# Optimization experiments

Hardware: AMD Instinct MI355X
Metric: run time of the kernel (lower is better)

The kernel has to match this reference:

```python
import jax, jax.numpy as jnp
import numpy as np
from jax import lax

HEADS = 8
EPS = 1e-5
B, HP, N = 16, 16, 256  # batch, patches per side, tokens


def _ln(x, w, b):
    m = x.mean(-1, keepdims=True)
    v = ((x - m) ** 2).mean(-1, keepdims=True)
    return (x - m) / jnp.sqrt(v + EPS) * w + b


def _mlp_block(x, n2w, n2b, f1w, f1b, f2w, f2b):
    h = _ln(x, n2w, n2b)
    h = jax.nn.gelu(h @ f1w.T + f1b, approximate=False)  # torch nn.GELU = exact erf
    return x + (h @ f2w.T + f2b)


def _stem_stage(x, params):
    def step(c, p):
        return _mlp_block(c, *p), None
    x, _ = lax.scan(step, x, params)
    return x


def _patch_merge(x, nw, nb, rw):
    # x: [B, N, s, s, C] -> [B, N, s/2, s/2, 2C]
    x = jnp.concatenate([x[..., 0::2, 0::2, :], x[..., 1::2, 0::2, :],
                         x[..., 0::2, 1::2, :], x[..., 1::2, 1::2, :]], axis=-1)
    return _ln(x, nw, nb) @ rw.T


def _main_block(x, p, rpe_index):
    n1w, n1b, qkvw, qkvb, rpb, pw, pb, n2w, n2b, f1w, f1b, f2w, f2b = p
    Bc, Nc, C = x.shape
    Dh = C // HEADS
    h = _ln(x, n1w, n1b)
    qkv = (h @ qkvw.T + qkvb).reshape(Bc, Nc, 3, HEADS, Dh)
    q, k, v = jnp.moveaxis(qkv, 2, 0)
    attn = jnp.einsum('bnhd,bmhd->bhnm', q * (Dh ** -0.5), k)
    # learned relative position bias gathered per (query, key) pair
    bias = rpb[rpe_index].reshape(Nc, Nc, HEADS).transpose(2, 0, 1)  # [H,N,N]
    attn = jax.nn.softmax((attn + bias[None]).astype(jnp.float32), axis=-1).astype(x.dtype)
    o = jnp.einsum('bhnm,bmhd->bnhd', attn, v).reshape(Bc, Nc, C)
    x = x + (o @ pw.T + pb)
    return _mlp_block(x, n2w, n2b, f1w, f1b, f2w, f2b)


def _forward(x, patch_w, patch_b, pnorm_w, pnorm_b,
             s0_n2w, s0_n2b, s0_fc1w, s0_fc1b, s0_fc2w, s0_fc2b,
             m0_nw, m0_nb, m0_rw,
             s1_n2w, s1_n2b, s1_fc1w, s1_fc1b, s1_fc2w, s1_fc2b,
             m1_nw, m1_nb, m1_rw, pos_embed,
             mb_n1w, mb_n1b, mb_qkvw, mb_qkvb, mb_rpb, mb_projw, mb_projb,
             mb_n2w, mb_n2b, mb_fc1w, mb_fc1b, mb_fc2w, mb_fc2b,
             fnorm_w, fnorm_b, rpe_index):
    Bc = x.shape[0]
    # PatchEmbed: 4x4/stride4 conv, regroup into [B, 256 patches, 4, 4, 128]
    h = lax.conv_general_dilated(x, patch_w, (4, 4), 'VALID',
                                 dimension_numbers=('NCHW', 'OIHW', 'NCHW'))
    h = h + patch_b[None, :, None, None]  # [B,128,64,64]
    h = h.reshape(Bc, 128, HP, 4, HP, 4).transpose(0, 2, 4, 3, 5, 1).reshape(Bc, N, 4, 4, 128)
    h = _ln(h, pnorm_w, pnorm_b)
    # stem stage 0 (8 MLP-only blocks, dim 128) + merge -> dim 256
    h = _stem_stage(h, (s0_n2w, s0_n2b, s0_fc1w, s0_fc1b, s0_fc2w, s0_fc2b))
    h = _patch_merge(h, m0_nw, m0_nb, m0_rw)  # [B,256,2,2,256]
    # stem stage 1 (8 MLP-only blocks, dim 256) + merge -> dim 512
    h = _stem_stage(h, (s1_n2w, s1_n2b, s1_fc1w, s1_fc1b, s1_fc2w, s1_fc2b))
    h = _patch_merge(h, m1_nw, m1_nb, m1_rw)  # [B,256,1,1,512]
    h = h[..., 0, 0, :] + pos_embed  # [B,256,512]
    # 20 main attention blocks with RPE
    def step(c, p):
        return _main_block(c, p, rpe_index), None
    h, _ = lax.scan(step, h, (mb_n1w, mb_n1b, mb_qkvw, mb_qkvb, mb_rpb,
                              mb_projw, mb_projb, mb_n2w, mb_n2b,
                              mb_fc1w, mb_fc1b, mb_fc2w, mb_fc2b))
    return _ln(h, fnorm_w, fnorm_b)


def _rpe_index():
    coords = np.stack(np.meshgrid(np.arange(HP), np.arange(HP), indexing='ij')).reshape(2, -1)
    rel = (coords[:, :, None] - coords[:, None, :]).transpose(1, 2, 0) + (HP - 1)
    return jnp.asarray((rel[..., 0] * (2 * HP - 1) + rel[..., 1]).reshape(-1), jnp.int32)


def setup_inputs() -> dict:
    key = jax.random.key(0)
    ks = iter(jax.random.split(key, 64))
    w = lambda shape: jax.random.normal(next(ks), shape, jnp.float32) * 0.02
    return {
        'x': jax.random.normal(next(ks), (B, 3, 256, 256), jnp.float32),
        'patch_w': w((128, 3, 4, 4)), 'patch_b': jnp.zeros(128),
        'pnorm_w': jnp.ones(128), 'pnorm_b': jnp.zeros(128),
        's0_n2w': jnp.ones((8, 128)), 's0_n2b': jnp.zeros((8, 128)),
        's0_fc1w': w((8, 384, 128)), 's0_fc1b': jnp.zeros((8, 384)),
        's0_fc2w': w((8, 128, 384)), 's0_fc2b': jnp.zeros((8, 128)),
        'm0_nw': jnp.ones(512), 'm0_nb': jnp.zeros(512), 'm0_rw': w((256, 512)),
        's1_n2w': jnp.ones((8, 256)), 's1_n2b': jnp.zeros((8, 256)),
        's1_fc1w': w((8, 768, 256)), 's1_fc1b': jnp.zeros((8, 768)),
        's1_fc2w': w((8, 256, 768)), 's1_fc2b': jnp.zeros((8, 256)),
        'm1_nw': jnp.ones(1024), 'm1_nb': jnp.zeros(1024), 'm1_rw': w((512, 1024)),
        'pos_embed': w((1, N, 512)),
        'mb_n1w': jnp.ones((20, 512)), 'mb_n1b': jnp.zeros((20, 512)),
        'mb_qkvw': w((20, 1536, 512)), 'mb_qkvb': jnp.zeros((20, 1536)),
        'mb_rpb': w((20, 961, 8)),
        'mb_projw': w((20, 512, 512)), 'mb_projb': jnp.zeros((20, 512)),
        'mb_n2w': jnp.ones((20, 512)), 'mb_n2b': jnp.zeros((20, 512)),
        'mb_fc1w': w((20, 2048, 512)), 'mb_fc1b': jnp.zeros((20, 2048)),
        'mb_fc2w': w((20, 512, 2048)), 'mb_fc2b': jnp.zeros((20, 512)),
        'fnorm_w': jnp.ones(512), 'fnorm_b': jnp.zeros(512),
        'rpe_index': _rpe_index(),
    }


def reference(x, patch_w, patch_b, pnorm_w, pnorm_b,
              s0_n2w, s0_n2b, s0_fc1w, s0_fc1b, s0_fc2w, s0_fc2b,
              m0_nw, m0_nb, m0_rw,
              s1_n2w, s1_n2b, s1_fc1w, s1_fc1b, s1_fc2w, s1_fc2b,
              m1_nw, m1_nb, m1_rw, pos_embed,
              mb_n1w, mb_n1b, mb_qkvw, mb_qkvb, mb_rpb, mb_projw, mb_projb,
              mb_n2w, mb_n2b, mb_fc1w, mb_fc1b, mb_fc2w, mb_fc2b,
              fnorm_w, fnorm_b, rpe_index):
    return _forward(x, patch_w, patch_b, pnorm_w, pnorm_b,
                    s0_n2w, s0_n2b, s0_fc1w, s0_fc1b, s0_fc2w, s0_fc2b,
                    m0_nw, m0_nb, m0_rw,
                    s1_n2w, s1_n2b, s1_fc1w, s1_fc1b, s1_fc2w, s1_fc2b,
                    m1_nw, m1_nb, m1_rw, pos_embed,
                    mb_n1w, mb_n1b, mb_qkvw, mb_qkvb, mb_rpb, mb_projw, mb_projb,
                    mb_n2w, mb_n2b, mb_fc1w, mb_fc1b, mb_fc2w, mb_fc2b,
                    fnorm_w, fnorm_b, rpe_index)
```

## Files before the change

kernel.cpp:

```cpp
#include <hip/hip_runtime.h>
#include <math.h>

#define EPSV 1e-5f

typedef __attribute__((ext_vector_type(8))) short bf16x8;
typedef __attribute__((ext_vector_type(4))) float f32x4;
typedef unsigned short ushort;

__device__ inline ushort f2bf(float x) {
  unsigned u = __builtin_bit_cast(unsigned, x);
  u += 0x7FFFu + ((u >> 16) & 1u);
  return (ushort)(u >> 16);
}

#define GLOAD16(lptr, gptr)                                              \
  __builtin_amdgcn_global_load_lds(                                      \
      (const __attribute__((address_space(1))) unsigned int*)(gptr),     \
      (__attribute__((address_space(3))) unsigned int*)(lptr), 16, 0, 0)

__global__ __launch_bounds__(256) void convh_kernel(
    const float* __restrict__ in, ushort* __restrict__ hi, int n4) {
  int i = blockIdx.x * 256 + threadIdx.x;
  if (i >= n4) return;
  float4 v = ((const float4*)in)[i];
  float vv[4] = {v.x, v.y, v.z, v.w};
  unsigned hw[4];
#pragma unroll
  for (int e = 0; e < 4; ++e) hw[e] = f2bf(vv[e]);
  ((uint2*)hi)[i] = make_uint2(hw[0] | (hw[1] << 16), hw[2] | (hw[3] << 16));
}

__global__ __launch_bounds__(256) void convmain_kernel(
    const float* __restrict__ src, ushort* __restrict__ dst, int perLayer4,
    int dstOff4, int n4) {
  int i = blockIdx.x * 256 + threadIdx.x;
  if (i >= n4) return;
  int l = i / perLayer4;
  int r = i - l * perLayer4;
  float4 v = ((const float4*)src)[i];
  float vv[4] = {v.x, v.y, v.z, v.w};
  unsigned hw[4];
#pragma unroll
  for (int e = 0; e < 4; ++e) hw[e] = f2bf(vv[e]);
  ((uint2*)dst)[(size_t)l * 786432 + dstOff4 + r] =
      make_uint2(hw[0] | (hw[1] << 16), hw[2] | (hw[3] << 16));
}

__global__ __launch_bounds__(256) void patch_ln2_kernel(
    const float* __restrict__ x, const float* __restrict__ pw,
    const float* __restrict__ pbias, const float* __restrict__ nw,
    const float* __restrict__ nb, float* __restrict__ out) {
  int bid = blockIdx.x;
  int b = bid >> 8, n = bid & 255;
  int py = (n >> 4) * 16, px0 = (n & 15) * 16;
  __shared__ float xin[3][16][16];
  __shared__ float wls[128][52];
  __shared__ float pbs[128];
  int tid = threadIdx.x;
  if (tid < 192) {
    int ci = tid / 64, rr = (tid % 64) >> 2, c4 = tid & 3;
    const float* src =
        x + ((size_t)(b * 3 + ci) * 256 + (py + rr)) * 256 + px0 + c4 * 4;
    *(float4*)&xin[ci][rr][c4 * 4] = *(const float4*)src;
  }
  for (int idx = tid; idx < 6144; idx += 256) {
    int c = idx / 48, q = idx % 48;
    wls[c][q] = pw[c * 48 + q];
  }
  if (tid < 128) pbs[tid] = pbias[tid];
  __syncthreads();

  int tt = tid >> 4, cg = tid & 15;
  int ii = tt >> 2, jj = tt & 3;
  float xv[48];
#pragma unroll
  for (int ci = 0; ci < 3; ++ci)
#pragma unroll
    for (int dy = 0; dy < 4; ++dy)
#pragma unroll
      for (int dx = 0; dx < 4; ++dx)
        xv[ci * 16 + dy * 4 + dx] = xin[ci][ii * 4 + dy][jj * 4 + dx];

  float o[8];
#pragma unroll
  for (int e = 0; e < 8; ++e) {
    int c = cg + e * 16;
    float a = pbs[c];
#pragma unroll
    for (int q4 = 0; q4 < 12; ++q4) {
      float4 w4 = *(const float4*)&wls[c][q4 * 4];
      a += w4.x * xv[q4 * 4] + w4.y * xv[q4 * 4 + 1] + w4.z * xv[q4 * 4 + 2] +
           w4.w * xv[q4 * 4 + 3];
    }
    o[e] = a;
  }
  float s = 0.f;
#pragma unroll
  for (int e = 0; e < 8; ++e) s += o[e];
#pragma unroll
  for (int off = 8; off > 0; off >>= 1) s += __shfl_xor(s, off, 16);
  float mean = s * (1.0f / 128.0f);
  float sq = 0.f;
#pragma unroll
  for (int e = 0; e < 8; ++e) {
    float d = o[e] - mean;
    sq += d * d;
  }
#pragma unroll
  for (int off = 8; off > 0; off >>= 1) sq += __shfl_xor(sq, off, 16);
  float rstd = rsqrtf(sq * (1.0f / 128.0f) + EPSV);
  size_t base = ((size_t)bid * 16 + tt) * 128;
#pragma unroll
  for (int e = 0; e < 8; ++e) {
    int c = cg + e * 16;
    out[base + c] = (o[e] - mean) * rstd * nw[c] + nb[c];
  }
}

template <int C>
__global__ __launch_bounds__(256) void lnC_kernel(
    const float* __restrict__ X, const float* __restrict__ w,
    const float* __restrict__ bb, ushort* __restrict__ outH) {
  constexpr int NV = C / 64;
  int wave = threadIdx.x >> 6, lane = threadIdx.x & 63;
  int row = blockIdx.x * 4 + wave;
  const float* xr = X + (size_t)row * C + lane * NV;
  float v[NV];
  if (NV == 2) {
    float2 t2 = *(const float2*)xr;
    v[0] = t2.x; v[1] = t2.y;
  } else {
#pragma unroll
    for (int q = 0; q < NV; q += 4) {
      float4 t4 = *(const float4*)(xr + q);
      v[q] = t4.x; v[q + 1] = t4.y; v[q + 2] = t4.z; v[q + 3] = t4.w;
    }
  }
  float s = 0.f;
#pragma unroll
  for (int q = 0; q < NV; ++q) s += v[q];
#pragma unroll
  for (int o = 32; o > 0; o >>= 1) s += __shfl_xor(s, o, 64);
  float mean = s * (1.0f / C);
  float sq = 0.f;
#pragma unroll
  for (int q = 0; q < NV; ++q) {
    float d = v[q] - mean;
    sq += d * d;
  }
#pragma unroll
  for (int o = 32; o > 0; o >>= 1) sq += __shfl_xor(sq, o, 64);
  float rstd = rsqrtf(sq * (1.0f / C) + EPSV);
#pragma unroll
  for (int q = 0; q < NV; ++q) {
    int c = lane * NV + q;
    outH[(size_t)row * C + c] = f2bf((v[q] - mean) * rstd * w[c] + bb[c]);
  }
}

template <int MODE>
__global__ __launch_bounds__(256) void merge_ln_kernel(
    const float* __restrict__ Xin, const float* __restrict__ nw,
    const float* __restrict__ nb, ushort* __restrict__ outH) {
  constexpr int CM = MODE ? 1024 : 512;
  constexpr int NE = CM / 256;
  int ot = blockIdx.x;
  int tid = threadIdx.x;
  __shared__ float redA[4];
  __shared__ float redB[4];

  float v[NE];
#pragma unroll
  for (int e = 0; e < NE; ++e) {
    int cp = tid + e * 256;
    if (MODE == 0) {
      int b = ot >> 10, r = ot & 1023;
      int n = r >> 2, di = (r >> 1) & 1, dj = r & 1;
      int q = cp >> 7, c = cp & 127;
      int i = 2 * di + (q & 1), j = 2 * dj + (q >> 1);
      v[e] = Xin[((b * 256 + n) * 16 + i * 4 + j) * 128 + c];
    } else {
      int b = ot >> 8, n = ot & 255;
      int q = cp >> 8, c = cp & 255;
      int di = q & 1, dj = q >> 1;
      v[e] = Xin[((b * 256 + n) * 4 + di * 2 + dj) * 256 + c];
    }
  }
  float s = 0.f;
#pragma unroll
  for (int e = 0; e < NE; ++e) s += v[e];
#pragma unroll
  for (int o = 32; o > 0; o >>= 1) s += __shfl_xor(s, o, 64);
  if ((tid & 63) == 0) redA[tid >> 6] = s;
  __syncthreads();
  float mean = (redA[0] + redA[1] + redA[2] + redA[3]) * (1.0f / CM);
  float sq = 0.f;
#pragma unroll
  for (int e = 0; e < NE; ++e) {
    float d = v[e] - mean;
    sq += d * d;
  }
#pragma unroll
  for (int o = 32; o > 0; o >>= 1) sq += __shfl_xor(sq, o, 64);
  if ((tid & 63) == 0) redB[tid >> 6] = sq;
  __syncthreads();
  float var = (redB[0] + redB[1] + redB[2] + redB[3]) * (1.0f / CM);
  float rstd = rsqrtf(var + EPSV);
#pragma unroll
  for (int e = 0; e < NE; ++e) {
    int cp = tid + e * 256;
    outH[(size_t)ot * CM + cp] = f2bf((v[e] - mean) * rstd * nw[cp] + nb[cp]);
  }
}

template <int EP, int BM>
__global__ __launch_bounds__(256) void mgemm4_kernel(
    const ushort* __restrict__ Ah, const ushort* __restrict__ Wh,
    const float* __restrict__ bias, const float* __restrict__ extra,
    float* __restrict__ outF, ushort* __restrict__ outH, int M, int N, int K) {
  constexpr int NI = BM / 32;
  constexpr int ASH = BM * 64;
  constexpr int LSZ = (ASH + 8192 > BM * 136) ? (ASH + 8192) : (BM * 136);
  __shared__ __align__(16) ushort Lds[LSZ];
  int nb = N >> 7;
  int bx = blockIdx.x % nb, by = blockIdx.x / nb;
  int tid = threadIdx.x;
  int wv = tid >> 6, lane = tid & 63;
  int srow = tid >> 3;
  int scol = ((tid & 7) ^ (srow & 7)) << 3;
  const ushort* aS = Ah + (size_t)(by * BM + srow) * K + scol;
  const ushort* wS = Wh + (size_t)(bx * 128 + srow) * K + scol;
  ushort* dA = Lds + wv * 512;
  ushort* dW = Lds + ASH + wv * 512;

  int wm = (wv >> 1) * (BM / 2), wn = (wv & 1) * 64;
  int fr = lane & 15, fq = lane >> 4;
  int rsw = fr & 7;

  f32x4 acc[NI][4];
#pragma unroll
  for (int i = 0; i < NI; ++i)
#pragma unroll
    for (int j = 0; j < 4; ++j) acc[i][j] = {0.f, 0.f, 0.f, 0.f};

  for (int k0 = 0; k0 < K; k0 += 64) {
#pragma unroll
    for (int q = 0; q < BM / 32; ++q)
      GLOAD16(dA + q * 2048, aS + (size_t)q * 32 * K + k0);
#pragma unroll
    for (int q = 0; q < 4; ++q)
      GLOAD16(dW + q * 2048, wS + (size_t)q * 32 * K + k0);
    __syncthreads();

#pragma unroll
    for (int kh = 0; kh < 2; ++kh) {
      bf16x8 fa[NI], fb[4];
#pragma unroll
      for (int i = 0; i < NI; ++i) {
        int row = wm + i * 16 + fr;
        fa[i] = *(const bf16x8*)(Lds + row * 64 + ((((kh << 2) + fq) ^ rsw) << 3));
      }
#pragma unroll
      for (int j = 0; j < 4; ++j) {
        int row = wn + j * 16 + fr;
        fb[j] = *(const bf16x8*)(Lds + ASH + row * 64 +
                                 ((((kh << 2) + fq) ^ rsw) << 3));
      }
#pragma unroll
      for (int i = 0; i < NI; ++i)
#pragma unroll
        for (int j = 0; j < 4; ++j)
          acc[i][j] = __builtin_amdgcn_mfma_f32_16x16x32_bf16(fa[i], fb[j],
                                                              acc[i][j], 0, 0,
                                                              0);
    }
    __syncthreads();
  }

  int row0 = by * BM;
  int col0 = bx * 128;
  if (EP == 3 || EP == 4) {
    ushort* LdsO = Lds;
#pragma unroll
    for (int j = 0; j < 4; ++j) {
      int col = wn + j * 16 + fr;
      float bvv = bias ? bias[col0 + col] : 0.f;
      bool sc = (EP == 4) && (col0 + col < 512);
#pragma unroll
      for (int i = 0; i < NI; ++i) {
#pragma unroll
        for (int e = 0; e < 4; ++e) {
          int rl = wm + i * 16 + fq * 4 + e;
          float o = acc[i][j][e] + bvv;
          if (EP == 3)
            o = 0.5f * o * (1.0f + erff(o * 0.70710678118654752f));
          else if (sc)
            o *= 0.125f;
          LdsO[rl * 136 + col] = f2bf(o);
        }
      }
    }
    __syncthreads();
#pragma unroll
    for (int p = 0; p < BM / 16; ++p) {
      int ch = p * 256 + tid;
      int r = ch >> 4, cc = (ch & 15) * 8;
      *(uint4*)&outH[(size_t)(row0 + r) * N + col0 + cc] =
          *(const uint4*)&LdsO[r * 136 + cc];
    }
  } else {
    float* LdsF = (float*)Lds;
    int strip = wv >> 1;
#pragma unroll
    for (int i = 0; i < NI; ++i) {
#pragma unroll
      for (int j = 0; j < 4; ++j) {
        int col = wn + j * 16 + fr;
        float bvv = bias ? bias[col0 + col] : 0.f;
#pragma unroll
        for (int e = 0; e < 4; ++e)
          LdsF[(strip * 16 + fq * 4 + e) * 136 + col] = acc[i][j][e] + bvv;
      }
      __syncthreads();
#pragma unroll
      for (int p = 0; p < 4; ++p) {
        int c = p * 256 + tid;
        int st = c >> 9;
        int rem = c & 511;
        int r = rem >> 5, cc = (rem & 31) * 4;
        int grow = row0 + st * (BM / 2) + i * 16 + r;
        float4 v = *(const float4*)&LdsF[(st * 16 + r) * 136 + cc];
        if (EP == 1) {
          float4 e4 =
              *(const float4*)&extra[(size_t)(grow & 255) * N + col0 + cc];
          v.x += e4.x; v.y += e4.y; v.z += e4.z; v.w += e4.w;
        } else if (EP == 2) {
          float4 e4 = *(const float4*)&extra[(size_t)grow * N + col0 + cc];
          v.x += e4.x; v.y += e4.y; v.z += e4.z; v.w += e4.w;
        }
        *(float4*)&outF[(size_t)grow * N + col0 + cc] = v;
      }
      __syncthreads();
    }
  }
}

__global__ __launch_bounds__(256) void attn_fused2_kernel(
    const ushort* __restrict__ qkvh, const float* __restrict__ rpb,
    const int* __restrict__ rpe, ushort* __restrict__ outH) {
  int bid = blockIdx.x;
  int qc = bid & 3, bh = bid >> 2;
  int b = bh >> 3, h = bh & 7;
  int n0 = qc * 64;
  int tid = threadIdx.x;
  int wv = tid >> 6, lane = tid & 63;
  int fr = lane & 15, fq = lane >> 4;
  __shared__ __align__(16) ushort Qs[64 * 64];
  __shared__ __align__(16) ushort Ks[256 * 64];
  __shared__ __align__(16) ushort Vt[64 * 256];
  __shared__ float rpbh[961];
  __shared__ float red[64][4];

  int srow = tid >> 3;
  int sc = ((tid & 7) ^ (srow & 7)) << 3;
  const ushort* Qg = qkvh + (size_t)(b * 256 + n0 + srow) * 1536 + h * 64 + sc;
  GLOAD16(Qs + wv * 512, Qg);
  GLOAD16(Qs + 2048 + wv * 512, Qg + (size_t)32 * 1536);
  const ushort* Kg = qkvh + (size_t)(b * 256 + srow) * 1536 + 512 + h * 64 + sc;
#pragma unroll
  for (int q = 0; q < 8; ++q)
    GLOAD16(Ks + q * 2048 + wv * 512, Kg + (size_t)q * 32 * 1536);
#pragma unroll
  for (int pass = 0; pass < 4; ++pass) {
    int m = pass * 64 + (tid >> 2);
    int sg = (tid & 3) * 16;
    const ushort* Vg = qkvh + (size_t)(b * 256 + m) * 1536 + 1024 + h * 64 + sg;
    ushort tmp[16];
    *(uint4*)tmp = *(const uint4*)Vg;
    *(uint4*)(tmp + 8) = *(const uint4*)(Vg + 8);
    int ch = m >> 3, ml = m & 7;
#pragma unroll
    for (int e = 0; e < 16; ++e) {
      int d = sg + e;
      int cs = (ch & 24) | ((ch & 7) ^ (d & 7));
      Vt[d * 256 + cs * 8 + ml] = tmp[e];
    }
  }
  for (int i = tid; i < 961; i += 256) rpbh[i] = rpb[i * 8 + h];
  __syncthreads();

  f32x4 acc[4][4];
#pragma unroll
  for (int i = 0; i < 4; ++i)
#pragma unroll
    for (int j = 0; j < 4; ++j) acc[i][j] = {0.f, 0.f, 0.f, 0.f};
#pragma unroll
  for (int kh = 0; kh < 2; ++kh) {
    bf16x8 fa[4], fb[4];
#pragma unroll
    for (int i = 0; i < 4; ++i) {
      int row = i * 16 + fr;
      fa[i] = *(const bf16x8*)(Qs + row * 64 +
                               ((((kh << 2) + fq) ^ (row & 7)) << 3));
    }
#pragma unroll
    for (int j = 0; j < 4; ++j) {
      int row = wv * 64 + j * 16 + fr;
      fb[j] = *(const bf16x8*)(Ks + row * 64 +
                               ((((kh << 2) + fq) ^ (row & 7)) << 3));
    }
#pragma unroll
    for (int i = 0; i < 4; ++i)
#pragma unroll
      for (int j = 0; j < 4; ++j)
        acc[i][j] = __builtin_amdgcn_mfma_f32_16x16x32_bf16(fa[i], fb[j],
                                                            acc[i][j], 0, 0, 0);
  }

  float sreg[4][4][4];
#pragma unroll
  for (int i = 0; i < 4; ++i)
#pragma unroll
    for (int e = 0; e < 4; ++e) {
      int n = n0 + i * 16 + fq * 4 + e;
#pragma unroll
      for (int j = 0; j < 4; ++j) {
        int m = wv * 64 + j * 16 + fr;
        sreg[i][j][e] = acc[i][j][e] + rpbh[rpe[n * 256 + m]];
      }
    }

  float rmax[4][4];
#pragma unroll
  for (int i = 0; i < 4; ++i)
#pragma unroll
    for (int e = 0; e < 4; ++e) {
      float mx = fmaxf(fmaxf(sreg[i][0][e], sreg[i][1][e]),
                       fmaxf(sreg[i][2][e], sreg[i][3][e]));
#pragma unroll
      for (int o = 8; o > 0; o >>= 1) mx = fmaxf(mx, __shfl_xor(mx, o, 16));
      if (fr == 0) red[i * 16 + fq * 4 + e][wv] = mx;
    }
  __syncthreads();
#pragma unroll
  for (int i = 0; i < 4; ++i)
#pragma unroll
    for (int e = 0; e < 4; ++e) {
      int row = i * 16 + fq * 4 + e;
      rmax[i][e] = fmaxf(fmaxf(red[row][0], red[row][1]),
                         fmaxf(red[row][2], red[row][3]));
    }
  __syncthreads();
  float rinv[4][4];
#pragma unroll
  for (int i = 0; i < 4; ++i)
#pragma unroll
    for (int e = 0; e < 4; ++e) {
      float sm = 0.f;
#pragma unroll
      for (int j = 0; j < 4; ++j) {
        sreg[i][j][e] = expf(sreg[i][j][e] - rmax[i][e]);
        sm += sreg[i][j][e];
      }
#pragma unroll
      for (int o = 8; o > 0; o >>= 1) sm += __shfl_xor(sm, o, 16);
      if (fr == 0) red[i * 16 + fq * 4 + e][wv] = sm;
    }
  __syncthreads();
#pragma unroll
  for (int i = 0; i < 4; ++i)
#pragma unroll
    for (int e = 0; e < 4; ++e) {
      int row = i * 16 + fq * 4 + e;
      rinv[i][e] =
          1.0f / (red[row][0] + red[row][1] + red[row][2] + red[row][3]);
    }
  ushort* Ps = Ks;
#pragma unroll
  for (int i = 0; i < 4; ++i)
#pragma unroll
    for (int e = 0; e < 4; ++e) {
      int qrow = i * 16 + fq * 4 + e;
#pragma unroll
      for (int j = 0; j < 4; ++j) {
        int m = wv * 64 + j * 16 + fr;
        int ch = m >> 3, t = m & 7;
        int cs = (ch & 24) | ((ch & 7) ^ (qrow & 7));
        Ps[qrow * 256 + cs * 8 + t] = f2bf(sreg[i][j][e] * rinv[i][e]);
      }
    }
  __syncthreads();

  f32x4 pacc[4];
#pragma unroll
  for (int i = 0; i < 4; ++i) pacc[i] = {0.f, 0.f, 0.f, 0.f};
  int dbase = wv * 16;
#pragma unroll
  for (int ks = 0; ks < 8; ++ks) {
    int ch = (ks << 2) + fq;
    bf16x8 fb;
    {
      int row = dbase + fr;
      int cs = (ch & 24) | ((ch & 7) ^ (row & 7));
      fb = *(const bf16x8*)(Vt + row * 256 + cs * 8);
    }
    bf16x8 fa[4];
#pragma unroll
    for (int i = 0; i < 4; ++i) {
      int row = i * 16 + fr;
      int cs = (ch & 24) | ((ch & 7) ^ (row & 7));
      fa[i] = *(const bf16x8*)(Ps + row * 256 + cs * 8);
    }
#pragma unroll
    for (int i = 0; i < 4; ++i)
      pacc[i] = __builtin_amdgcn_mfma_f32_16x16x32_bf16(fa[i], fb, pacc[i], 0,
                                                        0, 0);
  }
#pragma unroll
  for (int i = 0; i < 4; ++i)
#pragma unroll
    for (int e = 0; e < 4; ++e) {
      int q = i * 16 + fq * 4 + e;
      outH[(size_t)(b * 256 + n0 + q) * 512 + h * 64 + dbase + fr] =
          f2bf(pacc[i][e]);
    }
}

template <int HL>
__global__ __launch_bounds__(256) void ln512_kernel(
    const float* __restrict__ X, const float* __restrict__ w,
    const float* __restrict__ bb, float* __restrict__ outF,
    ushort* __restrict__ outH) {
  int row = blockIdx.x * 4 + (threadIdx.x >> 6);
  int t = threadIdx.x & 63;
  const float4* xr = (const float4*)(X + (size_t)row * 512);
  float4 v0 = xr[t * 2], v1 = xr[t * 2 + 1];
  float s = v0.x + v0.y + v0.z + v0.w + v1.x + v1.y + v1.z + v1.w;
#pragma unroll
  for (int o = 32; o > 0; o >>= 1) s += __shfl_xor(s, o, 64);
  float mean = s * (1.0f / 512.0f);
  float dv[8] = {v0.x - mean, v0.y - mean, v0.z - mean, v0.w - mean,
                 v1.x - mean, v1.y - mean, v1.z - mean, v1.w - mean};
  float sq = 0.f;
#pragma unroll
  for (int e = 0; e < 8; ++e) sq += dv[e] * dv[e];
#pragma unroll
  for (int o = 32; o > 0; o >>= 1) sq += __shfl_xor(sq, o, 64);
  float rstd = rsqrtf(sq * (1.0f / 512.0f) + EPSV);
  int c = t * 8;
  float ov[8];
#pragma unroll
  for (int e = 0; e < 8; ++e) ov[e] = dv[e] * rstd * w[c + e] + bb[c + e];
  if (HL == 0) {
    float4 o0 = {ov[0], ov[1], ov[2], ov[3]};
    float4 o1 = {ov[4], ov[5], ov[6], ov[7]};
    ((float4*)(outF + (size_t)row * 512))[t * 2] = o0;
    ((float4*)(outF + (size_t)row * 512))[t * 2 + 1] = o1;
  } else {
    __align__(16) ushort h8[8];
#pragma unroll
    for (int e = 0; e < 8; ++e) h8[e] = f2bf(ov[e]);
    *(bf16x8*)(outH + (size_t)row * 512 + c) = *(bf16x8*)h8;
  }
}

extern "C" void kernel_launch(void* const* d_in, const int* in_sizes, int n_in,
                              void* d_out, int out_size, void* d_ws,
                              size_t ws_size, hipStream_t stream) {
  const float* x = (const float*)d_in[0];
  const float* patch_w = (const float*)d_in[1];
  const float* patch_b = (const float*)d_in[2];
  const float* pnorm_w = (const float*)d_in[3];
  const float* pnorm_b = (const float*)d_in[4];
  const float* s0_n2w = (const float*)d_in[5];
  const float* s0_n2b = (const float*)d_in[6];
  const float* s0_f1w = (const float*)d_in[7];
  const float* s0_f1b = (const float*)d_in[8];
  const float* s0_f2w = (const float*)d_in[9];
  const float* s0_f2b = (const float*)d_in[10];
  const float* m0_nw = (const float*)d_in[11];
  const float* m0_nb = (const float*)d_in[12];
  const float* m0_rw = (const float*)d_in[13];
  const float* s1_n2w = (const float*)d_in[14];
  const float* s1_n2b = (const float*)d_in[15];
  const float* s1_f1w = (const float*)d_in[16];
  const float* s1_f1b = (const float*)d_in[17];
  const float* s1_f2w = (const float*)d_in[18];
  const float* s1_f2b = (const float*)d_in[19];
  const float* m1_nw = (const float*)d_in[20];
  const float* m1_nb = (const float*)d_in[21];
  const float* m1_rw = (const float*)d_in[22];
  const float* pos_embed = (const float*)d_in[23];
  const float* mb_n1w = (const float*)d_in[24];
  const float* mb_n1b = (const float*)d_in[25];
  const float* mb_qkvw = (const float*)d_in[26];
  const float* mb_qkvb = (const float*)d_in[27];
  const float* mb_rpb = (const float*)d_in[28];
  const float* mb_projw = (const float*)d_in[29];
  const float* mb_projb = (const float*)d_in[30];
  const float* mb_n2w = (const float*)d_in[31];
  const float* mb_n2b = (const float*)d_in[32];
  const float* mb_f1w = (const float*)d_in[33];
  const float* mb_f1b = (const float*)d_in[34];
  const float* mb_f2w = (const float*)d_in[35];
  const float* mb_f2b = (const float*)d_in[36];
  const float* fnorm_w = (const float*)d_in[37];
  const float* fnorm_b = (const float*)d_in[38];
  const int* rpe = (const int*)d_in[39];

  float* Xa = (float*)d_ws;
  ushort* BufB = (ushort*)(Xa + 8388608);
  ushort* BufC = (ushort*)(Xa + 12582912);
  ushort* Qkvh = BufC;
  ushort* F1h = BufC + 14680064;
  ushort* Wall = (ushort*)(Xa + 25165824);
  ushort* WallBig = (ushort*)(Xa + 27262976);

#define CONVH(src, cnt, dh)                                              \
  convh_kernel<<<((cnt) / 4 + 255) / 256, 256, 0, stream>>>(src, dh, (cnt) / 4)

  convmain_kernel<<<(20 * 196608 + 255) / 256, 256, 0, stream>>>(
      mb_qkvw, WallBig, 196608, 0, 20 * 196608);
  convmain_kernel<<<(20 * 65536 + 255) / 256, 256, 0, stream>>>(
      mb_projw, WallBig, 65536, 196608, 20 * 65536);
  convmain_kernel<<<(20 * 262144 + 255) / 256, 256, 0, stream>>>(
      mb_f1w, WallBig, 262144, 262144, 20 * 262144);
  convmain_kernel<<<(20 * 262144 + 255) / 256, 256, 0, stream>>>(
      mb_f2w, WallBig, 262144, 524288, 20 * 262144);

  patch_ln2_kernel<<<4096, 256, 0, stream>>>(x, patch_w, patch_b, pnorm_w,
                                             pnorm_b, Xa);

  CONVH(s0_f1w, 8 * 49152, Wall);
  CONVH(s0_f2w, 8 * 49152, Wall + 393216);
  for (int i = 0; i < 8; ++i) {
    lnC_kernel<128><<<65536 / 4, 256, 0, stream>>>(Xa, s0_n2w + i * 128,
                                                   s0_n2b + i * 128, BufB);
    mgemm4_kernel<3, 128><<<(65536 / 128) * (384 / 128), 256, 0, stream>>>(
        BufB, Wall + i * 49152, s0_f1b + i * 384, nullptr, nullptr, BufC,
        65536, 384, 128);
    mgemm4_kernel<2, 64><<<(65536 / 64) * (128 / 128), 256, 0, stream>>>(
        BufC, Wall + 393216 + i * 49152, s0_f2b + i * 128, Xa, Xa, nullptr,
        65536, 128, 384);
  }
  merge_ln_kernel<0><<<16384, 256, 0, stream>>>(Xa, m0_nw, m0_nb, BufB);
  CONVH(m0_rw, 131072, Wall);
  mgemm4_kernel<0, 128><<<(16384 / 128) * (256 / 128), 256, 0, stream>>>(
      BufB, Wall, nullptr, nullptr, Xa, nullptr, 16384, 256, 512);

  CONVH(s1_f1w, 8 * 196608, Wall);
  CONVH(s1_f2w, 8 * 196608, Wall + 1572864);
  for (int i = 0; i < 8; ++i) {
    lnC_kernel<256><<<16384 / 4, 256, 0, stream>>>(Xa, s1_n2w + i * 256,
                                                   s1_n2b + i * 256, BufB);
    mgemm4_kernel<3, 128><<<(16384 / 128) * (768 / 128), 256, 0, stream>>>(
        BufB, Wall + i * 196608, s1_f1b + i * 768, nullptr, nullptr, BufC,
        16384, 768, 256);
    mgemm4_kernel<2, 64><<<(16384 / 64) * (256 / 128), 256, 0, stream>>>(
        BufC, Wall + 1572864 + i * 196608, s1_f2b + i * 256, Xa, Xa, nullptr,
        16384, 256, 768);
  }
  merge_ln_kernel<1><<<4096, 256, 0, stream>>>(Xa, m1_nw, m1_nb, BufB);
  CONVH(m1_rw, 524288, Wall);
  mgemm4_kernel<1, 64><<<(4096 / 64) * (512 / 128), 256, 0, stream>>>(
      BufB, Wall, nullptr, pos_embed, Xa, nullptr, 4096, 512, 1024);

  for (int l = 0; l < 20; ++l) {
    ushort* Wl = WallBig + (size_t)l * 3145728;
    ln512_kernel<1><<<1024, 256, 0, stream>>>(Xa, mb_n1w + l * 512,
                                              mb_n1b + l * 512, nullptr, BufB);
    mgemm4_kernel<4, 64><<<(4096 / 64) * (1536 / 128), 256, 0, stream>>>(
        BufB, Wl, mb_qkvb + l * 1536, nullptr, nullptr, Qkvh, 4096, 1536,
        512);
    attn_fused2_kernel<<<512, 256, 0, stream>>>(Qkvh, mb_rpb + l * 7688, rpe,
                                                BufB);
    mgemm4_kernel<2, 64><<<(4096 / 64) * (512 / 128), 256, 0, stream>>>(
        BufB, Wl + 786432, mb_projb + l * 512, Xa, Xa, nullptr, 4096, 512,
        512);
    ln512_kernel<1><<<1024, 256, 0, stream>>>(Xa, mb_n2w + l * 512,
                                              mb_n2b + l * 512, nullptr, BufB);
    mgemm4_kernel<3, 128><<<(4096 / 128) * (2048 / 128), 256, 0, stream>>>(
        BufB, Wl + 1048576, mb_f1b + l * 2048, nullptr, nullptr, F1h, 4096,
        2048, 512);
    mgemm4_kernel<2, 64><<<(4096 / 64) * (512 / 128), 256, 0, stream>>>(
        F1h, Wl + 2097152, mb_f2b + l * 512, Xa, Xa, nullptr, 4096, 512,
        2048);
  }
  ln512_kernel<0><<<1024, 256, 0, stream>>>(Xa, fnorm_w, fnorm_b,
                                            (float*)d_out, nullptr);
}
```

Before: 3.531 ms.

## Fuse stem LayerNorm into FC1 GEMM with GELU epilogue

Replaces the separate LayerNorm kernel plus FC1 GEMM in both stem stages with a new kernel. It loads the fp32 activation tile into LDS, computes per-row mean and rstd, and applies normalization with bf16 conversion on the fly while building MFMA A-fragments. This removes the bf16 intermediate write and read and one launch per block. The cost is that each N-tile recomputes LN and re-reads fp32 X (3x or 6x redundancy), uses more LDS with smaller BM tiles, and does per-element conversion in the inner loop.

```diff
diff --git a/kernel.cpp b/kernel.cpp
--- a/kernel.cpp
+++ b/kernel.cpp
@@ -114,47 +114,6 @@
   for (int e = 0; e < 8; ++e) {
     int c = cg + e * 16;
     out[base + c] = (o[e] - mean) * rstd * nw[c] + nb[c];
-  }
-}
-
-template <int C>
-__global__ __launch_bounds__(256) void lnC_kernel(
-    const float* __restrict__ X, const float* __restrict__ w,
-    const float* __restrict__ bb, ushort* __restrict__ outH) {
-  constexpr int NV = C / 64;
-  int wave = threadIdx.x >> 6, lane = threadIdx.x & 63;
-  int row = blockIdx.x * 4 + wave;
-  const float* xr = X + (size_t)row * C + lane * NV;
-  float v[NV];
-  if (NV == 2) {
-    float2 t2 = *(const float2*)xr;
-    v[0] = t2.x; v[1] = t2.y;
-  } else {
-#pragma unroll
-    for (int q = 0; q < NV; q += 4) {
-      float4 t4 = *(const float4*)(xr + q);
-      v[q] = t4.x; v[q + 1] = t4.y; v[q + 2] = t4.z; v[q + 3] = t4.w;
-    }
-  }
-  float s = 0.f;
-#pragma unroll
-  for (int q = 0; q < NV; ++q) s += v[q];
-#pragma unroll
-  for (int o = 32; o > 0; o >>= 1) s += __shfl_xor(s, o, 64);
-  float mean = s * (1.0f / C);
-  float sq = 0.f;
-#pragma unroll
-  for (int q = 0; q < NV; ++q) {
-    float d = v[q] - mean;
-    sq += d * d;
-  }
-#pragma unroll
-  for (int o = 32; o > 0; o >>= 1) sq += __shfl_xor(sq, o, 64);
-  float rstd = rsqrtf(sq * (1.0f / C) + EPSV);
-#pragma unroll
-  for (int q = 0; q < NV; ++q) {
-    int c = lane * NV + q;
-    outH[(size_t)row * C + c] = f2bf((v[q] - mean) * rstd * w[c] + bb[c]);
   }
 }
 
@@ -342,6 +301,137 @@
       }
       __syncthreads();
     }
+  }
+}
+
+template <int C, int BM>
+__global__ __launch_bounds__(256) void mgemm5_kernel(
+    const float* __restrict__ X, const ushort* __restrict__ Wh,
+    const float* __restrict__ lnw, const float* __restrict__ lnb,
+    const float* __restrict__ bias, ushort* __restrict__ outH, int M, int N) {
+  constexpr int NI = BM / 32;
+  constexpr int CP = C + 4;
+  constexpr int XFSH = BM * CP * 2;
+  __shared__ __align__(16) ushort Lds[XFSH + 8192];
+  __shared__ float msh[BM], rsh[BM];
+  __shared__ float wch[C], bch[C];
+  float* Xf = (float*)Lds;
+  ushort* Wl = Lds + XFSH;
+  int nb = N >> 7;
+  int bx = blockIdx.x % nb, by = blockIdx.x / nb;
+  int tid = threadIdx.x;
+  int wv = tid >> 6, lane = tid & 63;
+  int fr = lane & 15, fq = lane >> 4;
+  int wm = (wv >> 1) * (BM / 2), wn = (wv & 1) * 64;
+
+  constexpr int NF4 = BM * C / 4;
+  for (int idx = tid; idx < NF4; idx += 256) {
+    int row = idx / (C / 4), c4 = idx % (C / 4);
+    float4 v = *(const float4*)(X + (size_t)(by * BM + row) * C + c4 * 4);
+    *(float4*)&Xf[row * CP + c4 * 4] = v;
+  }
+  for (int idx = tid; idx < C; idx += 256) {
+    wch[idx] = lnw[idx];
+    bch[idx] = lnb[idx];
+  }
+  __syncthreads();
+  if (tid < BM * 4) {
+    int row = tid >> 2, part = tid & 3;
+    const float* xr = &Xf[row * CP + part * (C / 4)];
+    float s = 0.f;
+#pragma unroll
+    for (int q = 0; q < C / 4; ++q) s += xr[q];
+    s += __shfl_xor(s, 1, 4);
+    s += __shfl_xor(s, 2, 4);
+    float mean = s * (1.0f / C);
+    float sq = 0.f;
+#pragma unroll
+    for (int q = 0; q < C / 4; ++q) {
+      float d = xr[q] - mean;
+      sq += d * d;
+    }
+    sq += __shfl_xor(sq, 1, 4);
+    sq += __shfl_xor(sq, 2, 4);
+    if (part == 0) {
+      msh[row] = mean;
+      rsh[row] = rsqrtf(sq * (1.0f / C) + EPSV);
+    }
+  }
+  __syncthreads();
+
+  int srow = tid >> 3;
+  int scol = ((tid & 7) ^ (srow & 7)) << 3;
+  const ushort* wS = Wh + (size_t)(bx * 128 + srow) * C + scol;
+  ushort* dW = Wl + wv * 512;
+
+  f32x4 acc[NI][4];
+#pragma unroll
+  for (int i = 0; i < NI; ++i)
+#pragma unroll
+    for (int j = 0; j < 4; ++j) acc[i][j] = {0.f, 0.f, 0.f, 0.f};
+
+  for (int k0 = 0; k0 < C; k0 += 64) {
+#pragma unroll
+    for (int q = 0; q < 4; ++q)
+      GLOAD16(dW + q * 2048, wS + (size_t)q * 32 * C + k0);
+    __syncthreads();
+#pragma unroll
+    for (int kh = 0; kh < 2; ++kh) {
+      bf16x8 fa[NI], fb[4];
+#pragma unroll
+      for (int i = 0; i < NI; ++i) {
+        int row = wm + i * 16 + fr;
+        int kof = k0 + ((kh << 2) + fq) * 8;
+        float mean = msh[row], rstd = rsh[row];
+        const float* xp = &Xf[row * CP + kof];
+        __align__(16) ushort tmp[8];
+#pragma unroll
+        for (int e = 0; e < 8; ++e)
+          tmp[e] = f2bf((xp[e] - mean) * rstd * wch[kof + e] + bch[kof + e]);
+        fa[i] = *(bf16x8*)tmp;
+      }
+#pragma unroll
+      for (int j = 0; j < 4; ++j) {
+        int row = wn + j * 16 + fr;
+        fb[j] = *(const bf16x8*)(Wl + row * 64 +
+                                 ((((kh << 2) + fq) ^ (row & 7)) << 3));
+      }
+#pragma unroll
+      for (int i = 0; i < NI; ++i)
+#pragma unroll
+        for (int j = 0; j < 4; ++j)
+          acc[i][j] = __builtin_amdgcn_mfma_f32_16x16x32_bf16(fa[i], fb[j],
+                                                              acc[i][j], 0, 0,
+                                                              0);
+    }
+    __syncthreads();
+  }
+
+  int row0 = by * BM;
+  int col0 = bx * 128;
+  ushort* LdsO = Lds;
+#pragma unroll
+  for (int j = 0; j < 4; ++j) {
+    int col = wn + j * 16 + fr;
+    float bvv = bias[col0 + col];
+#pragma unroll
+    for (int i = 0; i < NI; ++i) {
+#pragma unroll
+      for (int e = 0; e < 4; ++e) {
+        int rl = wm + i * 16 + fq * 4 + e;
+        float o = acc[i][j][e] + bvv;
+        o = 0.5f * o * (1.0f + erff(o * 0.70710678118654752f));
+        LdsO[rl * 136 + col] = f2bf(o);
+      }
+    }
+  }
+  __syncthreads();
+#pragma unroll
+  for (int p = 0; p < BM / 16; ++p) {
+    int ch = p * 256 + tid;
+    int r = ch >> 4, cc = (ch & 15) * 8;
+    *(uint4*)&outH[(size_t)(row0 + r) * N + col0 + cc] =
+        *(const uint4*)&LdsO[r * 136 + cc];
   }
 }
 
@@ -634,11 +724,9 @@
   CONVH(s0_f1w, 8 * 49152, Wall);
   CONVH(s0_f2w, 8 * 49152, Wall + 393216);
   for (int i = 0; i < 8; ++i) {
-    lnC_kernel<128><<<65536 / 4, 256, 0, stream>>>(Xa, s0_n2w + i * 128,
-                                                   s0_n2b + i * 128, BufB);
-    mgemm4_kernel<3, 128><<<(65536 / 128) * (384 / 128), 256, 0, stream>>>(
-        BufB, Wall + i * 49152, s0_f1b + i * 384, nullptr, nullptr, BufC,
-        65536, 384, 128);
+    mgemm5_kernel<128, 64><<<(65536 / 64) * (384 / 128), 256, 0, stream>>>(
+        Xa, Wall + i * 49152, s0_n2w + i * 128, s0_n2b + i * 128,
+        s0_f1b + i * 384, BufC, 65536, 384);
     mgemm4_kernel<2, 64><<<(65536 / 64) * (128 / 128), 256, 0, stream>>>(
         BufC, Wall + 393216 + i * 49152, s0_f2b + i * 128, Xa, Xa, nullptr,
         65536, 128, 384);
@@ -651,11 +739,9 @@
   CONVH(s1_f1w, 8 * 196608, Wall);
   CONVH(s1_f2w, 8 * 196608, Wall + 1572864);
   for (int i = 0; i < 8; ++i) {
-    lnC_kernel<256><<<16384 / 4, 256, 0, stream>>>(Xa, s1_n2w + i * 256,
-                                                   s1_n2b + i * 256, BufB);
-    mgemm4_kernel<3, 128><<<(16384 / 128) * (768 / 128), 256, 0, stream>>>(
-        BufB, Wall + i * 196608, s1_f1b + i * 768, nullptr, nullptr, BufC,
-        16384, 768, 256);
+    mgemm5_kernel<256, 32><<<(16384 / 32) * (768 / 128), 256, 0, stream>>>(
+        Xa, Wall + i * 196608, s1_n2w + i * 256, s1_n2b + i * 256,
+        s1_f1b + i * 768, BufC, 16384, 768);
     mgemm4_kernel<2, 64><<<(16384 / 64) * (256 / 128), 256, 0, stream>>>(
         BufC, Wall + 1572864 + i * 196608, s1_f2b + i * 256, Xa, Xa, nullptr,
         16384, 256, 768);
```

Result: slower. 3.668 ms (+3.9%).
